# Kernel tuning notes

Measured on AMD Instinct MI355X. Metric: run time of the kernel, lower is better.

The kernel has to match this reference:

```python
import jax, jax.numpy as jnp
import numpy as np

G, NPG = 256, 128          # graphs per batch, nodes per graph
N = G * NPG                # 32768 total nodes
E = 524288                 # total directed edges; first half 'in', second half 'out'
DIN, D = 128, 256          # input feature dim, hidden dim
R = 200                    # num relations
C = 2                      # num classes
EPS = 1e-5                 # batchnorm eps


def setup_inputs() -> dict:
    key = jax.random.key(0)
    ks = jax.random.split(key, 20)

    def w(k, shape):
        fan_in = shape[-2] if len(shape) >= 2 else shape[-1]
        return jax.random.normal(k, shape, jnp.float32) / np.float32(np.sqrt(fan_in))

    return {
        "x": jax.random.normal(ks[0], (N, DIN), jnp.float32),
        "rel_emb": w(ks[1], (R, DIN)),
        # conv1: DIN -> D
        "w_in1": w(ks[2], (DIN, D)), "w_out1": w(ks[3], (DIN, D)),
        "w_loop1": w(ks[4], (DIN, D)), "w_rel1": w(ks[5], (DIN, D)),
        "loop_rel1": w(ks[6], (1, DIN)),
        "bias1": jnp.zeros((D,), jnp.float32),
        "gamma1": jnp.ones((D,), jnp.float32), "beta1": jnp.zeros((D,), jnp.float32),
        # conv2..conv5 stacked: D -> D
        "W_in": w(ks[7], (4, D, D)), "W_out": w(ks[8], (4, D, D)),
        "W_loop": w(ks[9], (4, D, D)), "W_rel": w(ks[10], (4, D, D)),
        "Loop_rel": w(ks[11], (4, 1, D)),
        "Bias": jnp.zeros((4, D), jnp.float32),
        "Gamma": jnp.ones((4, D), jnp.float32), "Beta": jnp.zeros((4, D), jnp.float32),
        # head: concat2 => Linear(4*D, C)
        "lin_w": w(ks[12], (4 * D, C)), "lin_b": jnp.zeros((C,), jnp.float32),
        # graph data (int constants)
        "edge_index": jax.random.randint(ks[13], (2, E), 0, N),
        "edge_type": jax.random.randint(ks[14], (E,), 0, R),
        "batch": jnp.repeat(jnp.arange(G, dtype=jnp.int32), NPG),
        "rel_labels": jax.random.randint(ks[15], (G,), 0, R),
    }


def _compgcn_conv(x, rel, edge_index, edge_type,
                  w_in, w_out, w_loop, w_rel, loop_rel, bias, gamma, beta):
    """One CompGCNConv layer (opn='mult', dropout=identity/eval, BN with batch stats)."""
    n = x.shape[0]
    half = edge_index.shape[1] // 2

    def direction(idx, etype, W):
        src, dst = idx[0], idx[1]
        # symmetric normalization: deg^{-1/2}[src] * deg^{-1/2}[dst]
        deg = jax.ops.segment_sum(jnp.ones_like(src, jnp.float32), src, num_segments=n)
        dinv = jnp.where(deg > 0, deg ** -0.5, 0.0)
        norm = dinv[src] * dinv[dst]                       # [half]
        msg = ((x[src] * rel[etype]) @ W) * norm[:, None]  # [half, D]
        return jax.ops.segment_sum(msg, dst, num_segments=n)

    in_res = direction(edge_index[:, :half], edge_type[:half], w_in)
    out_res = direction(edge_index[:, half:], edge_type[half:], w_out)
    loop_res = (x * loop_rel) @ w_loop                     # self-loop, loop relation, no norm

    out = (in_res + out_res + loop_res) / 3.0 + bias
    mean = out.mean(axis=0)
    var = out.var(axis=0)
    out = (out - mean) / jnp.sqrt(var + EPS) * gamma + beta
    return jax.nn.relu(out), rel @ w_rel


def reference(x, rel_emb, w_in1, w_out1, w_loop1, w_rel1, loop_rel1, bias1, gamma1, beta1,
              W_in, W_out, W_loop, W_rel, Loop_rel, Bias, Gamma, Beta,
              lin_w, lin_b, edge_index, edge_type, batch, rel_labels):
    x, r = _compgcn_conv(x, rel_emb, edge_index, edge_type,
                         w_in1, w_out1, w_loop1, w_rel1, loop_rel1, bias1, gamma1, beta1)
    for l in range(4):  # conv2..conv5 (fixed small layer loop)
        x, r = _compgcn_conv(x, r, edge_index, edge_type,
                             W_in[l], W_out[l], W_loop[l], W_rel[l],
                             Loop_rel[l], Bias[l], Gamma[l], Beta[l])

    # per-graph head/tail nodes (first two nodes of each graph) via segment offsets
    counts = jax.ops.segment_sum(jnp.ones((x.shape[0],), jnp.float32), batch, num_segments=G)
    offsets = (jnp.cumsum(counts) - counts).astype(jnp.int32)
    h_batch = x[offsets]
    t_batch = x[offsets + 1]

    pooled = jax.ops.segment_sum(x, batch, num_segments=G) / counts[:, None]
    rel_embs = r[rel_labels]

    feats = jnp.concatenate([pooled, rel_embs, h_batch, t_batch], axis=1)  # concat2 path
    return feats @ lin_w + lin_b


if __name__ == "__main__":
    out = reference(**setup_inputs())
    print(out.shape, out.dtype)
```

## Files before the change

### kernel.cpp

```cpp
#include <hip/hip_runtime.h>

#define NN 32768
#define GG 256
#define NPGN 128
#define ET 524288
#define EH 262144
#define D1 128
#define D2 256
#define RR 200

typedef unsigned short u16;
typedef __attribute__((ext_vector_type(8))) short bf16x8;
typedef __attribute__((ext_vector_type(4))) float f32x4;
typedef __attribute__((ext_vector_type(8))) unsigned short u16x8;
typedef __attribute__((ext_vector_type(4))) unsigned short u16x4;

__device__ __forceinline__ float bf2f(u16 u) {
    union { unsigned int i; float f; } v; v.i = ((unsigned int)u) << 16; return v.f;
}
__device__ __forceinline__ u16 f2bf(float f) {
    union { unsigned int i; float f; } v; v.f = f;
    unsigned int x = v.i;
    return (u16)((x + 0x7fffu + ((x >> 16) & 1u)) >> 16);
}

__global__ void k_hist(const int* __restrict__ ei, int* __restrict__ hs_in,
                       int* __restrict__ hs_out, int* __restrict__ hd_in,
                       int* __restrict__ hd_out) {
    int e = blockIdx.x * blockDim.x + threadIdx.x;
    if (e >= ET) return;
    int s = ei[e], d = ei[ET + e];
    if (e < EH) { atomicAdd(&hs_in[s], 1);  atomicAdd(&hd_in[d], 1); }
    else        { atomicAdd(&hs_out[s], 1); atomicAdd(&hd_out[d], 1); }
}

__global__ void k_dinv(const int* __restrict__ hs_in, const int* __restrict__ hs_out,
                       float* __restrict__ dinv_in, float* __restrict__ dinv_out) {
    int n = blockIdx.x * blockDim.x + threadIdx.x;
    if (n >= NN) return;
    int a = hs_in[n], b = hs_out[n];
    dinv_in[n]  = a > 0 ? rsqrtf((float)a) : 0.f;
    dinv_out[n] = b > 0 ? rsqrtf((float)b) : 0.f;
}

__global__ __launch_bounds__(1024) void k_scan(const int* __restrict__ hist,
                                               int* __restrict__ off) {
    __shared__ int lds[1024];
    int t = threadIdx.x;
    int base = t * 32;
    int loc[32];
    int s = 0;
#pragma unroll
    for (int i = 0; i < 32; ++i) { loc[i] = s; s += hist[base + i]; }
    lds[t] = s;
    int tot = s;
    __syncthreads();
    for (int st = 1; st < 1024; st <<= 1) {
        int v = (t >= st) ? lds[t - st] : 0;
        __syncthreads();
        lds[t] += v;
        __syncthreads();
    }
    int excl = lds[t] - tot;
#pragma unroll
    for (int i = 0; i < 32; ++i) off[base + i] = excl + loc[i];
    if (t == 1023) off[NN] = lds[1023];
}

__global__ void k_fill(const int* __restrict__ ei, const int* __restrict__ et,
                       const float* __restrict__ dinv, const int* __restrict__ off,
                       int* __restrict__ cur, int* __restrict__ c_src,
                       int* __restrict__ c_et, float* __restrict__ c_norm, int eoff) {
    int e = blockIdx.x * blockDim.x + threadIdx.x;
    if (e >= EH) return;
    int s = ei[eoff + e], d = ei[ET + eoff + e], t = et[eoff + e];
    int slot = off[d] + atomicAdd(&cur[d], 1);
    c_src[slot] = s;
    c_et[slot] = t;
    c_norm[slot] = dinv[s] * dinv[d];
}

__global__ void k_convx(const float* __restrict__ in, u16* __restrict__ out, int n) {
    int i = blockIdx.x * blockDim.x + threadIdx.x;
    if (i < n) out[i] = f2bf(in[i]);
}

__global__ void k_prepw(const float* __restrict__ Wi, const float* __restrict__ Wo,
                        const float* __restrict__ Wl, const float* __restrict__ lr,
                        u16* __restrict__ WiT, u16* __restrict__ WoT,
                        u16* __restrict__ WlT, int K, int L) {
    int idx = blockIdx.x * blockDim.x + threadIdx.x;
    int per = L * K * 256;
    if (idx >= 3 * per) return;
    int fam = idx / per, rem = idx % per;
    int l = rem / (K * 256), rr = rem % (K * 256);
    int k = rr / 256, n = rr % 256;
    const float* src = fam == 0 ? Wi : fam == 1 ? Wo : Wl;
    float v = src[((size_t)l * K + k) * 256 + n];
    if (fam == 2) v *= lr[l * K + k];
    u16* dst = fam == 0 ? WiT : fam == 1 ? WoT : WlT;
    dst[((size_t)l * 256 + n) * K + k] = f2bf(v);
}

template <int K>
__global__ __launch_bounds__(256) void k_gather2(
    const u16* __restrict__ x, const u16* __restrict__ relb,
    const int* __restrict__ csI, const int* __restrict__ cetI,
    const float* __restrict__ cnI, const int* __restrict__ offI,
    const int* __restrict__ csO, const int* __restrict__ cetO,
    const float* __restrict__ cnO, const int* __restrict__ offO,
    u16* __restrict__ aggI, u16* __restrict__ aggO) {
    constexpr int LPN = K / 8;
    constexpr int NPB = 256 / LPN;
    const int dir = blockIdx.y;
    const int* __restrict__ cs  = dir ? csO : csI;
    const int* __restrict__ cet = dir ? cetO : cetI;
    const float* __restrict__ cn = dir ? cnO : cnI;
    const int* __restrict__ off = dir ? offO : offI;
    u16* __restrict__ agg = dir ? aggO : aggI;

    int node = blockIdx.x * NPB + (threadIdx.x / LPN);
    int lane = threadIdx.x % LPN;
    int c = lane * 8;
    int e0 = off[node], e1 = off[node + 1];
    float acc[8] = {};
    int e = e0;
    for (; e + 4 <= e1; e += 4) {
        int s0 = cs[e],     s1 = cs[e + 1], s2 = cs[e + 2], s3 = cs[e + 3];
        int t0 = cet[e],    t1 = cet[e + 1], t2 = cet[e + 2], t3 = cet[e + 3];
        float n0 = cn[e], n1 = cn[e + 1], n2 = cn[e + 2], n3 = cn[e + 3];
        u16x8 xa = *(const u16x8*)(x + (size_t)s0 * K + c);
        u16x8 xb = *(const u16x8*)(x + (size_t)s1 * K + c);
        u16x8 xc = *(const u16x8*)(x + (size_t)s2 * K + c);
        u16x8 xd = *(const u16x8*)(x + (size_t)s3 * K + c);
        u16x8 ra = *(const u16x8*)(relb + (size_t)t0 * K + c);
        u16x8 rb = *(const u16x8*)(relb + (size_t)t1 * K + c);
        u16x8 rc = *(const u16x8*)(relb + (size_t)t2 * K + c);
        u16x8 rd = *(const u16x8*)(relb + (size_t)t3 * K + c);
#pragma unroll
        for (int i = 0; i < 8; ++i)
            acc[i] += n0 * bf2f(xa[i]) * bf2f(ra[i]) + n1 * bf2f(xb[i]) * bf2f(rb[i])
                    + n2 * bf2f(xc[i]) * bf2f(rc[i]) + n3 * bf2f(xd[i]) * bf2f(rd[i]);
    }
    for (; e < e1; ++e) {
        int s0 = cs[e], t0 = cet[e]; float n0 = cn[e];
        u16x8 xa = *(const u16x8*)(x + (size_t)s0 * K + c);
        u16x8 ra = *(const u16x8*)(relb + (size_t)t0 * K + c);
#pragma unroll
        for (int i = 0; i < 8; ++i) acc[i] += n0 * bf2f(xa[i]) * bf2f(ra[i]);
    }
    u16x8 o;
#pragma unroll
    for (int i = 0; i < 8; ++i) o[i] = f2bf(acc[i]);
    *(u16x8*)(agg + (size_t)node * K + c) = o;
}

__device__ __forceinline__ void stage_tile(const u16* __restrict__ src, int baseRow,
                                           int K, int kk, u16* lds, int wave, int lane) {
#pragma unroll
    for (int i = 0; i < 2; ++i) {
        int chunk = wave * 2 + i;
        int row = chunk * 16 + (lane >> 2);
        const u16* g = src + (size_t)(baseRow + row) * K + kk + (lane & 3) * 8;
        u16* l = lds + chunk * 512;
        __builtin_amdgcn_global_load_lds((const __attribute__((address_space(1))) void*)g,
                                         (__attribute__((address_space(3))) void*)l,
                                         16, 0, 0);
    }
}

template <int K>
__global__ __launch_bounds__(256) void k_gemm_mfma(
    const u16* __restrict__ A1, const u16* __restrict__ A2, const u16* __restrict__ A3,
    const u16* __restrict__ W1, const u16* __restrict__ W2, const u16* __restrict__ W3,
    const float* __restrict__ bias, float* __restrict__ C, float* __restrict__ bnsums) {
    __shared__ u16 As_s[2][128 * 32];
    __shared__ u16 Ws_s[2][128 * 32];
    const int tid = threadIdx.x;
    const int wave = tid >> 6, lane = tid & 63;
    const int q = lane >> 4, r = lane & 15;
    const int rowBlk = blockIdx.x * 128;
    const int colBlk = blockIdx.y * 128;
    const int rowBase = rowBlk + (wave & 1) * 64;
    const int colBase = colBlk + (wave >> 1) * 64;

    f32x4 zero = {0.f, 0.f, 0.f, 0.f};
    f32x4 acc[4][4];
#pragma unroll
    for (int i = 0; i < 4; ++i)
#pragma unroll
        for (int j = 0; j < 4; ++j) acc[i][j] = zero;

    const u16* As[3] = {A1, A2, A3};
    const u16* Ws[3] = {W1, W2, W3};
    constexpr int SPS = K / 32;
    constexpr int TOT = 3 * SPS;

    stage_tile(As[0], rowBlk, K, 0, As_s[0], wave, lane);
    stage_tile(Ws[0], colBlk, K, 0, Ws_s[0], wave, lane);

    for (int s = 0; s < TOT; ++s) {
        __syncthreads();
        if (s + 1 < TOT) {
            int seg = (s + 1) / SPS;
            int kk  = ((s + 1) % SPS) * 32;
            stage_tile(As[seg], rowBlk, K, kk, As_s[(s + 1) & 1], wave, lane);
            stage_tile(Ws[seg], colBlk, K, kk, Ws_s[(s + 1) & 1], wave, lane);
        }
        const u16* al = As_s[s & 1] + (wave & 1) * 64 * 32;
        const u16* wl = Ws_s[s & 1] + (wave >> 1) * 64 * 32;
        bf16x8 a[4], b[4];
#pragma unroll
        for (int t = 0; t < 4; ++t) {
            a[t] = *(const bf16x8*)(al + (t * 16 + r) * 32 + q * 8);
            b[t] = *(const bf16x8*)(wl + (t * 16 + r) * 32 + q * 8);
        }
#pragma unroll
        for (int tm = 0; tm < 4; ++tm)
#pragma unroll
            for (int tn = 0; tn < 4; ++tn)
                acc[tm][tn] = __builtin_amdgcn_mfma_f32_16x16x32_bf16(
                    a[tm], b[tn], acc[tm][tn], 0, 0, 0);
    }

#pragma unroll
    for (int tn = 0; tn < 4; ++tn) {
        int col = colBase + tn * 16 + r;
        float bv = bias[col];
        float sv = 0.f, qv = 0.f;
#pragma unroll
        for (int tm = 0; tm < 4; ++tm) {
#pragma unroll
            for (int reg = 0; reg < 4; ++reg) {
                int row = rowBase + tm * 16 + q * 4 + reg;
                float v = acc[tm][tn][reg] / 3.0f + bv;
                C[(size_t)row * 256 + col] = v;
                sv += v; qv += v * v;
            }
        }
        sv += __shfl_xor(sv, 16); sv += __shfl_xor(sv, 32);
        qv += __shfl_xor(qv, 16); qv += __shfl_xor(qv, 32);
        if (q == 0) {
            atomicAdd(&bnsums[col], sv);
            atomicAdd(&bnsums[256 + col], qv);
        }
    }
}

__global__ __launch_bounds__(256) void k_gemm_rel(
    const float* __restrict__ A, const float* __restrict__ W,
    float* __restrict__ C, u16* __restrict__ Cb, int M, int K) {
    __shared__ float As[16][68];
    __shared__ float Wshm[16][68];
    const int tid = threadIdx.x;
    const int tx = tid & 15, ty = tid >> 4;
    const int arow = tid >> 2;
    const int akc  = (tid & 3) << 2;
    const int wk   = tid >> 4;
    const int wn0  = (tid & 15) << 2;
    const int rowBase = blockIdx.x << 6;
    const int colBase = blockIdx.y << 6;
    float acc[4][4] = {};
    for (int k0 = 0; k0 < K; k0 += 16) {
        float4 av = make_float4(0.f, 0.f, 0.f, 0.f);
        int rr = rowBase + arow;
        if (rr < M) av = *(const float4*)(A + (size_t)rr * K + k0 + akc);
        As[akc + 0][arow] = av.x;
        As[akc + 1][arow] = av.y;
        As[akc + 2][arow] = av.z;
        As[akc + 3][arow] = av.w;
        float4 wv = *(const float4*)(W + (size_t)(k0 + wk) * D2 + colBase + wn0);
        Wshm[wk][wn0 + 0] = wv.x;
        Wshm[wk][wn0 + 1] = wv.y;
        Wshm[wk][wn0 + 2] = wv.z;
        Wshm[wk][wn0 + 3] = wv.w;
        __syncthreads();
#pragma unroll
        for (int kk = 0; kk < 16; ++kk) {
            float a0 = As[kk][(ty << 2) + 0], a1 = As[kk][(ty << 2) + 1];
            float a2 = As[kk][(ty << 2) + 2], a3 = As[kk][(ty << 2) + 3];
            float w0 = Wshm[kk][(tx << 2) + 0], w1 = Wshm[kk][(tx << 2) + 1];
            float w2 = Wshm[kk][(tx << 2) + 2], w3 = Wshm[kk][(tx << 2) + 3];
            acc[0][0] += a0 * w0; acc[0][1] += a0 * w1; acc[0][2] += a0 * w2; acc[0][3] += a0 * w3;
            acc[1][0] += a1 * w0; acc[1][1] += a1 * w1; acc[1][2] += a1 * w2; acc[1][3] += a1 * w3;
            acc[2][0] += a2 * w0; acc[2][1] += a2 * w1; acc[2][2] += a2 * w2; acc[2][3] += a2 * w3;
            acc[3][0] += a3 * w0; acc[3][1] += a3 * w1; acc[3][2] += a3 * w2; acc[3][3] += a3 * w3;
        }
        __syncthreads();
    }
#pragma unroll
    for (int i = 0; i < 4; ++i) {
        int rr = rowBase + (ty << 2) + i;
        if (rr >= M) continue;
        float* cp = C + (size_t)rr * D2 + colBase + (tx << 2);
        u16* cb = Cb + (size_t)rr * D2 + colBase + (tx << 2);
        cp[0] = acc[i][0]; cp[1] = acc[i][1]; cp[2] = acc[i][2]; cp[3] = acc[i][3];
        cb[0] = f2bf(acc[i][0]); cb[1] = f2bf(acc[i][1]);
        cb[2] = f2bf(acc[i][2]); cb[3] = f2bf(acc[i][3]);
    }
}

__global__ void k_bnapply(const float4* __restrict__ h4, const float* __restrict__ sums,
                          const float* __restrict__ gamma, const float* __restrict__ beta,
                          u16x4* __restrict__ xb4) {
    int idx = blockIdx.x * blockDim.x + threadIdx.x;
    int f0 = (idx & 63) << 2;
    float4 v = h4[idx];
    u16x4 o;
    float vv[4] = {v.x, v.y, v.z, v.w};
#pragma unroll
    for (int i = 0; i < 4; ++i) {
        int f = f0 + i;
        float mean = sums[f] * (1.0f / NN);
        float var  = sums[256 + f] * (1.0f / NN) - mean * mean;
        float inv  = 1.0f / sqrtf(var + 1e-5f);
        float t = (vv[i] - mean) * inv * gamma[f] + beta[f];
        o[i] = f2bf(t > 0.f ? t : 0.f);
    }
    xb4[idx] = o;
}

__global__ void k_feats(const u16* __restrict__ x, const float* __restrict__ rel,
                        const int* __restrict__ rel_labels, float* __restrict__ feats) {
    int g = blockIdx.x, f = threadIdx.x;
    const u16* xg = x + (size_t)g * NPGN * D2;
    float s = 0.f;
#pragma unroll 8
    for (int n = 0; n < NPGN; ++n) s += bf2f(xg[(size_t)n * D2 + f]);
    float* fg = feats + (size_t)g * 1024;
    fg[f]       = s * (1.0f / NPGN);
    fg[256 + f] = rel[(size_t)rel_labels[g] * D2 + f];
    fg[512 + f] = bf2f(xg[f]);
    fg[768 + f] = bf2f(xg[D2 + f]);
}

__global__ void k_head(const float* __restrict__ feats, const float* __restrict__ lw,
                       const float* __restrict__ lb, float* __restrict__ out) {
    int g = blockIdx.x, t = threadIdx.x;
    __shared__ float s0[256], s1[256];
    float a0 = 0.f, a1 = 0.f;
#pragma unroll
    for (int j = 0; j < 4; ++j) {
        int k = t * 4 + j;
        float fv = feats[(size_t)g * 1024 + k];
        a0 += fv * lw[k * 2 + 0];
        a1 += fv * lw[k * 2 + 1];
    }
    s0[t] = a0; s1[t] = a1;
    __syncthreads();
    for (int s = 128; s > 0; s >>= 1) {
        if (t < s) { s0[t] += s0[t + s]; s1[t] += s1[t + s]; }
        __syncthreads();
    }
    if (t == 0) {
        out[g * 2 + 0] = s0[0] + lb[0];
        out[g * 2 + 1] = s1[0] + lb[1];
    }
}

extern "C" void kernel_launch(void* const* d_in, const int* in_sizes, int n_in,
                              void* d_out, int out_size, void* d_ws, size_t ws_size,
                              hipStream_t stream) {
    const float* x0   = (const float*)d_in[0];
    const float* rel0 = (const float*)d_in[1];
    const int* edge_index = (const int*)d_in[20];
    const int* edge_type  = (const int*)d_in[21];
    const int* rel_labels = (const int*)d_in[23];
    float* out = (float*)d_out;

    float* ws = (float*)d_ws;
    float* h     = ws;
    float* relA  = h + (size_t)NN * 256;
    float* relB  = relA + (size_t)RR * 256;
    float* dinv_in  = relB + (size_t)RR * 256;
    float* dinv_out = dinv_in + NN;
    float* cnorm_in  = dinv_out + NN;
    float* cnorm_out = cnorm_in + EH;
    float* bnsums    = cnorm_out + EH;
    float* feats     = bnsums + 512;
    int* csrc_in  = (int*)(feats + GG * 1024);
    int* cet_in   = csrc_in + EH;
    int* csrc_out = cet_in + EH;
    int* cet_out  = csrc_out + EH;
    int* off_in   = cet_out + EH;
    int* off_out  = off_in + NN + 8;
    int* hs_in    = off_out + NN + 8;
    int* hs_out   = hs_in + NN;
    int* hd_in    = hs_out + NN;
    int* hd_out   = hd_in + NN;
    int* cur_in   = hd_out + NN;
    int* cur_out  = cur_in + NN;
    u16* xbf0 = (u16*)(cur_out + NN);
    u16* xbfA = xbf0 + (size_t)NN * 128;
    u16* aggI = xbfA + (size_t)NN * 256;
    u16* aggO = aggI + (size_t)NN * 256;
    u16* wt0  = aggO + (size_t)NN * 256;
    u16* wtS  = wt0 + 3 * 256 * 128;
    u16* relbf = wtS + 12 * 65536;

    hipMemsetAsync(hs_in, 0, 6 * NN * sizeof(int), stream);
    k_hist<<<ET / 256, 256, 0, stream>>>(edge_index, hs_in, hs_out, hd_in, hd_out);
    k_dinv<<<NN / 256, 256, 0, stream>>>(hs_in, hs_out, dinv_in, dinv_out);
    k_scan<<<1, 1024, 0, stream>>>(hd_in, off_in);
    k_scan<<<1, 1024, 0, stream>>>(hd_out, off_out);
    k_fill<<<EH / 256, 256, 0, stream>>>(edge_index, edge_type, dinv_in, off_in,
                                         cur_in, csrc_in, cet_in, cnorm_in, 0);
    k_fill<<<EH / 256, 256, 0, stream>>>(edge_index, edge_type, dinv_out, off_out,
                                         cur_out, csrc_out, cet_out, cnorm_out, EH);
    k_convx<<<(NN * D1) / 256, 256, 0, stream>>>(x0, xbf0, NN * D1);
    k_convx<<<(RR * D1 + 255) / 256, 256, 0, stream>>>(rel0, relbf, RR * D1);
    k_prepw<<<(3 * D1 * 256) / 256, 256, 0, stream>>>(
        (const float*)d_in[2], (const float*)d_in[3], (const float*)d_in[4],
        (const float*)d_in[6], wt0, wt0 + 256 * D1, wt0 + 2 * 256 * D1, D1, 1);
    k_prepw<<<(3 * 4 * D2 * 256) / 256, 256, 0, stream>>>(
        (const float*)d_in[10], (const float*)d_in[11], (const float*)d_in[12],
        (const float*)d_in[14], wtS, wtS + 4 * 65536, wtS + 8 * 65536, D2, 4);

    const float* rc = rel0; float* rn = relA;

    for (int l = 0; l < 5; ++l) {
        const int K = (l == 0) ? D1 : D2;
        const u16* xb = (l == 0) ? xbf0 : xbfA;
        const u16 *WiT, *WoT, *WlT;
        const float *Wr, *bias, *gamma, *beta;
        if (l == 0) {
            WiT = wt0; WoT = wt0 + 256 * D1; WlT = wt0 + 2 * 256 * D1;
            Wr = (const float*)d_in[5];
            bias  = (const float*)d_in[7];
            gamma = (const float*)d_in[8];
            beta  = (const float*)d_in[9];
        } else {
            int m = l - 1;
            WiT = wtS + (size_t)m * 65536;
            WoT = wtS + (size_t)(4 + m) * 65536;
            WlT = wtS + (size_t)(8 + m) * 65536;
            Wr = (const float*)d_in[13] + (size_t)m * D2 * D2;
            bias  = (const float*)d_in[15] + (size_t)m * D2;
            gamma = (const float*)d_in[16] + (size_t)m * D2;
            beta  = (const float*)d_in[17] + (size_t)m * D2;
        }

        if (K == D1) {
            dim3 ggr(NN / 16, 2);
            k_gather2<D1><<<ggr, 256, 0, stream>>>(xb, relbf, csrc_in, cet_in,
                cnorm_in, off_in, csrc_out, cet_out, cnorm_out, off_out, aggI, aggO);
        } else {
            dim3 ggr(NN / 8, 2);
            k_gather2<D2><<<ggr, 256, 0, stream>>>(xb, relbf, csrc_in, cet_in,
                cnorm_in, off_in, csrc_out, cet_out, cnorm_out, off_out, aggI, aggO);
        }
        hipMemsetAsync(bnsums, 0, 512 * sizeof(float), stream);
        dim3 ggrid(NN / 128, 2);
        if (K == D1) k_gemm_mfma<D1><<<ggrid, 256, 0, stream>>>(aggI, aggO, xb, WiT, WoT, WlT, bias, h, bnsums);
        else         k_gemm_mfma<D2><<<ggrid, 256, 0, stream>>>(aggI, aggO, xb, WiT, WoT, WlT, bias, h, bnsums);
        k_bnapply<<<(NN * 256 / 4) / 256, 256, 0, stream>>>((const float4*)h, bnsums,
                                                            gamma, beta, (u16x4*)xbfA);
        k_gemm_rel<<<dim3(4, 4), 256, 0, stream>>>(rc, Wr, rn, relbf, RR, K);
        const float* nr = rn;
        rn = (l == 0) ? relB : (float*)rc;
        rc = nr;
    }

    k_feats<<<GG, 256, 0, stream>>>(xbfA, rc, rel_labels, feats);
    k_head<<<GG, 256, 0, stream>>>(feats, (const float*)d_in[18],
                                   (const float*)d_in[19], out);
}
```

Before: 829.5 us.

## Degree-sort CSR nodes, split gather over columns, shrink GEMM tile, store bf16 pre-BN

```diff
diff --git a/kernel.cpp b/kernel.cpp
--- a/kernel.cpp
+++ b/kernel.cpp
@@ -13,7 +13,6 @@
 typedef __attribute__((ext_vector_type(8))) short bf16x8;
 typedef __attribute__((ext_vector_type(4))) float f32x4;
 typedef __attribute__((ext_vector_type(8))) unsigned short u16x8;
-typedef __attribute__((ext_vector_type(4))) unsigned short u16x4;
 
 __device__ __forceinline__ float bf2f(u16 u) {
     union { unsigned int i; float f; } v; v.i = ((unsigned int)u) << 16; return v.f;
@@ -41,6 +40,44 @@
     int a = hs_in[n], b = hs_out[n];
     dinv_in[n]  = a > 0 ? rsqrtf((float)a) : 0.f;
     dinv_out[n] = b > 0 ? rsqrtf((float)b) : 0.f;
+}
+
+__global__ void k_deghist(const int* __restrict__ hdI, const int* __restrict__ hdO,
+                          int* __restrict__ dh) {
+    int n = blockIdx.x * blockDim.x + threadIdx.x;
+    if (n >= NN) return;
+    atomicAdd(&dh[min(hdI[n], 63)], 1);
+    atomicAdd(&dh[64 + min(hdO[n], 63)], 1);
+}
+
+__global__ void k_scan64(const int* __restrict__ dh, int* __restrict__ dstart) {
+    int dir = threadIdx.x;
+    if (dir >= 2) return;
+    int s = 0;
+    for (int i = 0; i < 64; ++i) { dstart[dir * 64 + i] = s; s += dh[dir * 64 + i]; }
+}
+
+__global__ void k_place(const int* __restrict__ hdI, const int* __restrict__ hdO,
+                        const int* __restrict__ dstart, int* __restrict__ dcur,
+                        int* __restrict__ permI, int* __restrict__ permO,
+                        int* __restrict__ rankI, int* __restrict__ rankO) {
+    int n = blockIdx.x * blockDim.x + threadIdx.x;
+    if (n >= NN) return;
+    int dI = min(hdI[n], 63);
+    int rI = dstart[dI] + atomicAdd(&dcur[dI], 1);
+    permI[rI] = n; rankI[n] = rI;
+    int dO = min(hdO[n], 63);
+    int rO = dstart[64 + dO] + atomicAdd(&dcur[64 + dO], 1);
+    permO[rO] = n; rankO[n] = rO;
+}
+
+__global__ void k_degsorted(const int* __restrict__ permI, const int* __restrict__ permO,
+                            const int* __restrict__ hdI, const int* __restrict__ hdO,
+                            int* __restrict__ degSI, int* __restrict__ degSO) {
+    int i = blockIdx.x * blockDim.x + threadIdx.x;
+    if (i >= NN) return;
+    degSI[i] = hdI[permI[i]];
+    degSO[i] = hdO[permO[i]];
 }
 
 __global__ __launch_bounds__(1024) void k_scan(const int* __restrict__ hist,
@@ -68,13 +105,14 @@
 }
 
 __global__ void k_fill(const int* __restrict__ ei, const int* __restrict__ et,
-                       const float* __restrict__ dinv, const int* __restrict__ off,
-                       int* __restrict__ cur, int* __restrict__ c_src,
-                       int* __restrict__ c_et, float* __restrict__ c_norm, int eoff) {
+                       const float* __restrict__ dinv, const int* __restrict__ offS,
+                       const int* __restrict__ rank, int* __restrict__ cur,
+                       int* __restrict__ c_src, int* __restrict__ c_et,
+                       float* __restrict__ c_norm, int eoff) {
     int e = blockIdx.x * blockDim.x + threadIdx.x;
     if (e >= EH) return;
     int s = ei[eoff + e], d = ei[ET + eoff + e], t = et[eoff + e];
-    int slot = off[d] + atomicAdd(&cur[d], 1);
+    int slot = offS[rank[d]] + atomicAdd(&cur[d], 1);
     c_src[slot] = s;
     c_et[slot] = t;
     c_norm[slot] = dinv[s] * dinv[d];
@@ -103,31 +141,33 @@
 }
 
 template <int K>
-__global__ __launch_bounds__(256) void k_gather2(
+__global__ __launch_bounds__(256) void k_gather4(
     const u16* __restrict__ x, const u16* __restrict__ relb,
     const int* __restrict__ csI, const int* __restrict__ cetI,
     const float* __restrict__ cnI, const int* __restrict__ offI,
     const int* __restrict__ csO, const int* __restrict__ cetO,
     const float* __restrict__ cnO, const int* __restrict__ offO,
-    u16* __restrict__ aggI, u16* __restrict__ aggO) {
-    constexpr int LPN = K / 8;
-    constexpr int NPB = 256 / LPN;
+    const int* __restrict__ permI, const int* __restrict__ permO,
+    u16* __restrict__ aggI, u16* __restrict__ aggO, float* __restrict__ bnsums) {
+    if (blockIdx.x == 0 && blockIdx.y == 0 && blockIdx.z == 0 && threadIdx.x < 128)
+        ((float4*)bnsums)[threadIdx.x] = make_float4(0.f, 0.f, 0.f, 0.f);
     const int dir = blockIdx.y;
-    const int* __restrict__ cs  = dir ? csO : csI;
-    const int* __restrict__ cet = dir ? cetO : cetI;
+    const int* __restrict__ cs   = dir ? csO : csI;
+    const int* __restrict__ cet  = dir ? cetO : cetI;
     const float* __restrict__ cn = dir ? cnO : cnI;
-    const int* __restrict__ off = dir ? offO : offI;
+    const int* __restrict__ off  = dir ? offO : offI;
+    const int* __restrict__ perm = dir ? permO : permI;
     u16* __restrict__ agg = dir ? aggO : aggI;
 
-    int node = blockIdx.x * NPB + (threadIdx.x / LPN);
-    int lane = threadIdx.x % LPN;
-    int c = lane * 8;
-    int e0 = off[node], e1 = off[node + 1];
+    int idx = blockIdx.x * 32 + (threadIdx.x >> 3);
+    int node = perm[idx];
+    int c = blockIdx.z * 64 + (threadIdx.x & 7) * 8;
+    int e0 = off[idx], e1 = off[idx + 1];
     float acc[8] = {};
     int e = e0;
     for (; e + 4 <= e1; e += 4) {
-        int s0 = cs[e],     s1 = cs[e + 1], s2 = cs[e + 2], s3 = cs[e + 3];
-        int t0 = cet[e],    t1 = cet[e + 1], t2 = cet[e + 2], t3 = cet[e + 3];
+        int s0 = cs[e],  s1 = cs[e + 1],  s2 = cs[e + 2],  s3 = cs[e + 3];
+        int t0 = cet[e], t1 = cet[e + 1], t2 = cet[e + 2], t3 = cet[e + 3];
         float n0 = cn[e], n1 = cn[e + 1], n2 = cn[e + 2], n3 = cn[e + 3];
         u16x8 xa = *(const u16x8*)(x + (size_t)s0 * K + c);
         u16x8 xb = *(const u16x8*)(x + (size_t)s1 * K + c);
@@ -155,39 +195,35 @@
     *(u16x8*)(agg + (size_t)node * K + c) = o;
 }
 
-__device__ __forceinline__ void stage_tile(const u16* __restrict__ src, int baseRow,
-                                           int K, int kk, u16* lds, int wave, int lane) {
-#pragma unroll
-    for (int i = 0; i < 2; ++i) {
-        int chunk = wave * 2 + i;
-        int row = chunk * 16 + (lane >> 2);
-        const u16* g = src + (size_t)(baseRow + row) * K + kk + (lane & 3) * 8;
-        u16* l = lds + chunk * 512;
-        __builtin_amdgcn_global_load_lds((const __attribute__((address_space(1))) void*)g,
-                                         (__attribute__((address_space(3))) void*)l,
-                                         16, 0, 0);
-    }
+__device__ __forceinline__ void stage16(const u16* __restrict__ src, int baseRow,
+                                        int K, int kk, u16* lds, int chunk, int lane) {
+    int row = chunk * 16 + (lane >> 2);
+    int ks  = (lane & 3) ^ ((lane >> 2) & 3);
+    const u16* g = src + (size_t)(baseRow + row) * K + kk + ks * 8;
+    __builtin_amdgcn_global_load_lds((const __attribute__((address_space(1))) void*)g,
+                                     (__attribute__((address_space(3))) void*)(lds + chunk * 512),
+                                     16, 0, 0);
 }
 
 template <int K>
-__global__ __launch_bounds__(256) void k_gemm_mfma(
+__global__ __launch_bounds__(256, 4) void k_gemm_mfma(
     const u16* __restrict__ A1, const u16* __restrict__ A2, const u16* __restrict__ A3,
     const u16* __restrict__ W1, const u16* __restrict__ W2, const u16* __restrict__ W3,
-    const float* __restrict__ bias, float* __restrict__ C, float* __restrict__ bnsums) {
-    __shared__ u16 As_s[2][128 * 32];
+    const float* __restrict__ bias, u16* __restrict__ hb, float* __restrict__ bnsums) {
+    __shared__ u16 As_s[2][64 * 32];
     __shared__ u16 Ws_s[2][128 * 32];
     const int tid = threadIdx.x;
     const int wave = tid >> 6, lane = tid & 63;
     const int q = lane >> 4, r = lane & 15;
-    const int rowBlk = blockIdx.x * 128;
+    const int rowBlk = blockIdx.x * 64;
     const int colBlk = blockIdx.y * 128;
-    const int rowBase = rowBlk + (wave & 1) * 64;
+    const int rowBase = rowBlk + (wave & 1) * 32;
     const int colBase = colBlk + (wave >> 1) * 64;
 
     f32x4 zero = {0.f, 0.f, 0.f, 0.f};
-    f32x4 acc[4][4];
-#pragma unroll
-    for (int i = 0; i < 4; ++i)
+    f32x4 acc[2][4];
+#pragma unroll
+    for (int i = 0; i < 2; ++i)
 #pragma unroll
         for (int j = 0; j < 4; ++j) acc[i][j] = zero;
 
@@ -196,27 +232,29 @@
     constexpr int SPS = K / 32;
     constexpr int TOT = 3 * SPS;
 
-    stage_tile(As[0], rowBlk, K, 0, As_s[0], wave, lane);
-    stage_tile(Ws[0], colBlk, K, 0, Ws_s[0], wave, lane);
-
+    stage16(As[0], rowBlk, K, 0, As_s[0], wave, lane);
+    stage16(Ws[0], colBlk, K, 0, Ws_s[0], 2 * wave, lane);
+    stage16(Ws[0], colBlk, K, 0, Ws_s[0], 2 * wave + 1, lane);
+
+    const int sw = (q ^ (r & 3)) * 8;
     for (int s = 0; s < TOT; ++s) {
         __syncthreads();
         if (s + 1 < TOT) {
             int seg = (s + 1) / SPS;
             int kk  = ((s + 1) % SPS) * 32;
-            stage_tile(As[seg], rowBlk, K, kk, As_s[(s + 1) & 1], wave, lane);
-            stage_tile(Ws[seg], colBlk, K, kk, Ws_s[(s + 1) & 1], wave, lane);
+            stage16(As[seg], rowBlk, K, kk, As_s[(s + 1) & 1], wave, lane);
+            stage16(Ws[seg], colBlk, K, kk, Ws_s[(s + 1) & 1], 2 * wave, lane);
+            stage16(Ws[seg], colBlk, K, kk, Ws_s[(s + 1) & 1], 2 * wave + 1, lane);
         }
-        const u16* al = As_s[s & 1] + (wave & 1) * 64 * 32;
+        const u16* al = As_s[s & 1] + (wave & 1) * 32 * 32;
         const u16* wl = Ws_s[s & 1] + (wave >> 1) * 64 * 32;
-        bf16x8 a[4], b[4];
-#pragma unroll
-        for (int t = 0; t < 4; ++t) {
-            a[t] = *(const bf16x8*)(al + (t * 16 + r) * 32 + q * 8);
-            b[t] = *(const bf16x8*)(wl + (t * 16 + r) * 32 + q * 8);
-        }
-#pragma unroll
-        for (int tm = 0; tm < 4; ++tm)
+        bf16x8 a[2], b[4];
+#pragma unroll
+        for (int t = 0; t < 2; ++t) a[t] = *(const bf16x8*)(al + (t * 16 + r) * 32 + sw);
+#pragma unroll
+        for (int t = 0; t < 4; ++t) b[t] = *(const bf16x8*)(wl + (t * 16 + r) * 32 + sw);
+#pragma unroll
+        for (int tm = 0; tm < 2; ++tm)
 #pragma unroll
             for (int tn = 0; tn < 4; ++tn)
                 acc[tm][tn] = __builtin_amdgcn_mfma_f32_16x16x32_bf16(
@@ -229,12 +267,12 @@
         float bv = bias[col];
         float sv = 0.f, qv = 0.f;
 #pragma unroll
-        for (int tm = 0; tm < 4; ++tm) {
+        for (int tm = 0; tm < 2; ++tm) {
 #pragma unroll
             for (int reg = 0; reg < 4; ++reg) {
                 int row = rowBase + tm * 16 + q * 4 + reg;
-                float v = acc[tm][tn][reg] / 3.0f + bv;
-                C[(size_t)row * 256 + col] = v;
+                float v = acc[tm][tn][reg] * (1.0f / 3.0f) + bv;
+                hb[(size_t)row * 256 + col] = f2bf(v);
                 sv += v; qv += v * v;
             }
         }
@@ -300,24 +338,23 @@
     }
 }
 
-__global__ void k_bnapply(const float4* __restrict__ h4, const float* __restrict__ sums,
+__global__ void k_bnapply(const u16x8* __restrict__ hb8, const float* __restrict__ sums,
                           const float* __restrict__ gamma, const float* __restrict__ beta,
-                          u16x4* __restrict__ xb4) {
+                          u16x8* __restrict__ xb8) {
     int idx = blockIdx.x * blockDim.x + threadIdx.x;
-    int f0 = (idx & 63) << 2;
-    float4 v = h4[idx];
-    u16x4 o;
-    float vv[4] = {v.x, v.y, v.z, v.w};
-#pragma unroll
-    for (int i = 0; i < 4; ++i) {
+    int f0 = (idx & 31) << 3;
+    u16x8 v = hb8[idx];
+    u16x8 o;
+#pragma unroll
+    for (int i = 0; i < 8; ++i) {
         int f = f0 + i;
         float mean = sums[f] * (1.0f / NN);
         float var  = sums[256 + f] * (1.0f / NN) - mean * mean;
         float inv  = 1.0f / sqrtf(var + 1e-5f);
-        float t = (vv[i] - mean) * inv * gamma[f] + beta[f];
+        float t = (bf2f(v[i]) - mean) * inv * gamma[f] + beta[f];
         o[i] = f2bf(t > 0.f ? t : 0.f);
     }
-    xb4[idx] = o;
+    xb8[idx] = o;
 }
 
 __global__ void k_feats(const u16* __restrict__ x, const float* __restrict__ rel,
@@ -369,8 +406,7 @@
     float* out = (float*)d_out;
 
     float* ws = (float*)d_ws;
-    float* h     = ws;
-    float* relA  = h + (size_t)NN * 256;
+    float* relA  = ws;
     float* relB  = relA + (size_t)RR * 256;
     float* dinv_in  = relB + (size_t)RR * 256;
     float* dinv_out = dinv_in + NN;
@@ -382,31 +418,46 @@
     int* cet_in   = csrc_in + EH;
     int* csrc_out = cet_in + EH;
     int* cet_out  = csrc_out + EH;
-    int* off_in   = cet_out + EH;
-    int* off_out  = off_in + NN + 8;
-    int* hs_in    = off_out + NN + 8;
+    int* offS_in  = cet_out + EH;
+    int* offS_out = offS_in + NN + 8;
+    int* permI    = offS_out + NN + 8;
+    int* permO    = permI + NN;
+    int* rankI    = permO + NN;
+    int* rankO    = rankI + NN;
+    int* degSI    = rankO + NN;
+    int* degSO    = degSI + NN;
+    int* dstart   = degSO + NN;
+    int* hs_in    = dstart + 128;
     int* hs_out   = hs_in + NN;
     int* hd_in    = hs_out + NN;
     int* hd_out   = hd_in + NN;
     int* cur_in   = hd_out + NN;
     int* cur_out  = cur_in + NN;
-    u16* xbf0 = (u16*)(cur_out + NN);
+    int* dh       = cur_out + NN;
+    int* dcur     = dh + 128;
+    u16* xbf0 = (u16*)(dcur + 128);
     u16* xbfA = xbf0 + (size_t)NN * 128;
     u16* aggI = xbfA + (size_t)NN * 256;
     u16* aggO = aggI + (size_t)NN * 256;
-    u16* wt0  = aggO + (size_t)NN * 256;
+    u16* hb   = aggO + (size_t)NN * 256;
+    u16* wt0  = hb + (size_t)NN * 256;
     u16* wtS  = wt0 + 3 * 256 * 128;
     u16* relbf = wtS + 12 * 65536;
 
-    hipMemsetAsync(hs_in, 0, 6 * NN * sizeof(int), stream);
+    hipMemsetAsync(hs_in, 0, (6 * NN + 256) * sizeof(int), stream);
     k_hist<<<ET / 256, 256, 0, stream>>>(edge_index, hs_in, hs_out, hd_in, hd_out);
     k_dinv<<<NN / 256, 256, 0, stream>>>(hs_in, hs_out, dinv_in, dinv_out);
-    k_scan<<<1, 1024, 0, stream>>>(hd_in, off_in);
-    k_scan<<<1, 1024, 0, stream>>>(hd_out, off_out);
-    k_fill<<<EH / 256, 256, 0, stream>>>(edge_index, edge_type, dinv_in, off_in,
-                                         cur_in, csrc_in, cet_in, cnorm_in, 0);
-    k_fill<<<EH / 256, 256, 0, stream>>>(edge_index, edge_type, dinv_out, off_out,
-                                         cur_out, csrc_out, cet_out, cnorm_out, EH);
+    k_deghist<<<NN / 256, 256, 0, stream>>>(hd_in, hd_out, dh);
+    k_scan64<<<1, 64, 0, stream>>>(dh, dstart);
+    k_place<<<NN / 256, 256, 0, stream>>>(hd_in, hd_out, dstart, dcur,
+                                          permI, permO, rankI, rankO);
+    k_degsorted<<<NN / 256, 256, 0, stream>>>(permI, permO, hd_in, hd_out, degSI, degSO);
+    k_scan<<<1, 1024, 0, stream>>>(degSI, offS_in);
+    k_scan<<<1, 1024, 0, stream>>>(degSO, offS_out);
+    k_fill<<<EH / 256, 256, 0, stream>>>(edge_index, edge_type, dinv_in, offS_in,
+                                         rankI, cur_in, csrc_in, cet_in, cnorm_in, 0);
+    k_fill<<<EH / 256, 256, 0, stream>>>(edge_index, edge_type, dinv_out, offS_out,
+                                         rankO, cur_out, csrc_out, cet_out, cnorm_out, EH);
     k_convx<<<(NN * D1) / 256, 256, 0, stream>>>(x0, xbf0, NN * D1);
     k_convx<<<(RR * D1 + 255) / 256, 256, 0, stream>>>(rel0, relbf, RR * D1);
     k_prepw<<<(3 * D1 * 256) / 256, 256, 0, stream>>>(
@@ -440,21 +491,18 @@
             beta  = (const float*)d_in[17] + (size_t)m * D2;
         }
 
-        if (K == D1) {
-            dim3 ggr(NN / 16, 2);
-            k_gather2<D1><<<ggr, 256, 0, stream>>>(xb, relbf, csrc_in, cet_in,
-                cnorm_in, off_in, csrc_out, cet_out, cnorm_out, off_out, aggI, aggO);
-        } else {
-            dim3 ggr(NN / 8, 2);
-            k_gather2<D2><<<ggr, 256, 0, stream>>>(xb, relbf, csrc_in, cet_in,
-                cnorm_in, off_in, csrc_out, cet_out, cnorm_out, off_out, aggI, aggO);
-        }
-        hipMemsetAsync(bnsums, 0, 512 * sizeof(float), stream);
-        dim3 ggrid(NN / 128, 2);
-        if (K == D1) k_gemm_mfma<D1><<<ggrid, 256, 0, stream>>>(aggI, aggO, xb, WiT, WoT, WlT, bias, h, bnsums);
-        else         k_gemm_mfma<D2><<<ggrid, 256, 0, stream>>>(aggI, aggO, xb, WiT, WoT, WlT, bias, h, bnsums);
-        k_bnapply<<<(NN * 256 / 4) / 256, 256, 0, stream>>>((const float4*)h, bnsums,
-                                                            gamma, beta, (u16x4*)xbfA);
+        dim3 ggr(NN / 32, 2, K / 64);
+        if (K == D1) k_gather4<D1><<<ggr, 256, 0, stream>>>(xb, relbf,
+            csrc_in, cet_in, cnorm_in, offS_in, csrc_out, cet_out, cnorm_out, offS_out,
+            permI, permO, aggI, aggO, bnsums);
+        else         k_gather4<D2><<<ggr, 256, 0, stream>>>(xb, relbf,
+            csrc_in, cet_in, cnorm_in, offS_in, csrc_out, cet_out, cnorm_out, offS_out,
+            permI, permO, aggI, aggO, bnsums);
+        dim3 ggrid(NN / 64, 2);
+        if (K == D1) k_gemm_mfma<D1><<<ggrid, 256, 0, stream>>>(aggI, aggO, xb, WiT, WoT, WlT, bias, hb, bnsums);
+        else         k_gemm_mfma<D2><<<ggrid, 256, 0, stream>>>(aggI, aggO, xb, WiT, WoT, WlT, bias, hb, bnsums);
+        k_bnapply<<<(NN * 256 / 8) / 256, 256, 0, stream>>>((const u16x8*)hb, bnsums,
+                                                            gamma, beta, (u16x8*)xbfA);
         k_gemm_rel<<<dim3(4, 4), 256, 0, stream>>>(rc, Wr, rn, relbf, RR, K);
         const float* nr = rn;
         rn = (l == 0) ? relB : (float*)rc;
```

Measured after the change: 1.314 ms. +58.4%, slower.

## Store GEMM output as bf16, swizzle LDS tiles, fold bnsums zeroing into gather

Applied to the files above, without the earlier changes.

```diff
diff --git a/kernel.cpp b/kernel.cpp
--- a/kernel.cpp
+++ b/kernel.cpp
@@ -13,7 +13,6 @@
 typedef __attribute__((ext_vector_type(8))) short bf16x8;
 typedef __attribute__((ext_vector_type(4))) float f32x4;
 typedef __attribute__((ext_vector_type(8))) unsigned short u16x8;
-typedef __attribute__((ext_vector_type(4))) unsigned short u16x4;
 
 __device__ __forceinline__ float bf2f(u16 u) {
     union { unsigned int i; float f; } v; v.i = ((unsigned int)u) << 16; return v.f;
@@ -109,7 +108,9 @@
     const float* __restrict__ cnI, const int* __restrict__ offI,
     const int* __restrict__ csO, const int* __restrict__ cetO,
     const float* __restrict__ cnO, const int* __restrict__ offO,
-    u16* __restrict__ aggI, u16* __restrict__ aggO) {
+    u16* __restrict__ aggI, u16* __restrict__ aggO, float* __restrict__ bnsums) {
+    if (blockIdx.x == 0 && blockIdx.y == 0 && threadIdx.x < 128)
+        ((float4*)bnsums)[threadIdx.x] = make_float4(0.f, 0.f, 0.f, 0.f);
     constexpr int LPN = K / 8;
     constexpr int NPB = 256 / LPN;
     const int dir = blockIdx.y;
@@ -126,8 +127,8 @@
     float acc[8] = {};
     int e = e0;
     for (; e + 4 <= e1; e += 4) {
-        int s0 = cs[e],     s1 = cs[e + 1], s2 = cs[e + 2], s3 = cs[e + 3];
-        int t0 = cet[e],    t1 = cet[e + 1], t2 = cet[e + 2], t3 = cet[e + 3];
+        int s0 = cs[e],  s1 = cs[e + 1],  s2 = cs[e + 2],  s3 = cs[e + 3];
+        int t0 = cet[e], t1 = cet[e + 1], t2 = cet[e + 2], t3 = cet[e + 3];
         float n0 = cn[e], n1 = cn[e + 1], n2 = cn[e + 2], n3 = cn[e + 3];
         u16x8 xa = *(const u16x8*)(x + (size_t)s0 * K + c);
         u16x8 xb = *(const u16x8*)(x + (size_t)s1 * K + c);
@@ -155,25 +156,21 @@
     *(u16x8*)(agg + (size_t)node * K + c) = o;
 }
 
-__device__ __forceinline__ void stage_tile(const u16* __restrict__ src, int baseRow,
-                                           int K, int kk, u16* lds, int wave, int lane) {
-#pragma unroll
-    for (int i = 0; i < 2; ++i) {
-        int chunk = wave * 2 + i;
-        int row = chunk * 16 + (lane >> 2);
-        const u16* g = src + (size_t)(baseRow + row) * K + kk + (lane & 3) * 8;
-        u16* l = lds + chunk * 512;
-        __builtin_amdgcn_global_load_lds((const __attribute__((address_space(1))) void*)g,
-                                         (__attribute__((address_space(3))) void*)l,
-                                         16, 0, 0);
-    }
+__device__ __forceinline__ void stage16(const u16* __restrict__ src, int baseRow,
+                                        int K, int kk, u16* lds, int chunk, int lane) {
+    int row = chunk * 16 + (lane >> 2);
+    int ks  = (lane & 3) ^ ((lane >> 2) & 3);
+    const u16* g = src + (size_t)(baseRow + row) * K + kk + ks * 8;
+    __builtin_amdgcn_global_load_lds((const __attribute__((address_space(1))) void*)g,
+                                     (__attribute__((address_space(3))) void*)(lds + chunk * 512),
+                                     16, 0, 0);
 }
 
 template <int K>
 __global__ __launch_bounds__(256) void k_gemm_mfma(
     const u16* __restrict__ A1, const u16* __restrict__ A2, const u16* __restrict__ A3,
     const u16* __restrict__ W1, const u16* __restrict__ W2, const u16* __restrict__ W3,
-    const float* __restrict__ bias, float* __restrict__ C, float* __restrict__ bnsums) {
+    const float* __restrict__ bias, u16* __restrict__ hb, float* __restrict__ bnsums) {
     __shared__ u16 As_s[2][128 * 32];
     __shared__ u16 Ws_s[2][128 * 32];
     const int tid = threadIdx.x;
@@ -196,24 +193,29 @@
     constexpr int SPS = K / 32;
     constexpr int TOT = 3 * SPS;
 
-    stage_tile(As[0], rowBlk, K, 0, As_s[0], wave, lane);
-    stage_tile(Ws[0], colBlk, K, 0, Ws_s[0], wave, lane);
-
+    stage16(As[0], rowBlk, K, 0, As_s[0], 2 * wave, lane);
+    stage16(As[0], rowBlk, K, 0, As_s[0], 2 * wave + 1, lane);
+    stage16(Ws[0], colBlk, K, 0, Ws_s[0], 2 * wave, lane);
+    stage16(Ws[0], colBlk, K, 0, Ws_s[0], 2 * wave + 1, lane);
+
+    const int sw = (q ^ (r & 3)) * 8;
     for (int s = 0; s < TOT; ++s) {
         __syncthreads();
         if (s + 1 < TOT) {
             int seg = (s + 1) / SPS;
             int kk  = ((s + 1) % SPS) * 32;
-            stage_tile(As[seg], rowBlk, K, kk, As_s[(s + 1) & 1], wave, lane);
-            stage_tile(Ws[seg], colBlk, K, kk, Ws_s[(s + 1) & 1], wave, lane);
+            stage16(As[seg], rowBlk, K, kk, As_s[(s + 1) & 1], 2 * wave, lane);
+            stage16(As[seg], rowBlk, K, kk, As_s[(s + 1) & 1], 2 * wave + 1, lane);
+            stage16(Ws[seg], colBlk, K, kk, Ws_s[(s + 1) & 1], 2 * wave, lane);
+            stage16(Ws[seg], colBlk, K, kk, Ws_s[(s + 1) & 1], 2 * wave + 1, lane);
         }
         const u16* al = As_s[s & 1] + (wave & 1) * 64 * 32;
         const u16* wl = Ws_s[s & 1] + (wave >> 1) * 64 * 32;
         bf16x8 a[4], b[4];
 #pragma unroll
         for (int t = 0; t < 4; ++t) {
-            a[t] = *(const bf16x8*)(al + (t * 16 + r) * 32 + q * 8);
-            b[t] = *(const bf16x8*)(wl + (t * 16 + r) * 32 + q * 8);
+            a[t] = *(const bf16x8*)(al + (t * 16 + r) * 32 + sw);
+            b[t] = *(const bf16x8*)(wl + (t * 16 + r) * 32 + sw);
         }
 #pragma unroll
         for (int tm = 0; tm < 4; ++tm)
@@ -233,8 +235,8 @@
 #pragma unroll
             for (int reg = 0; reg < 4; ++reg) {
                 int row = rowBase + tm * 16 + q * 4 + reg;
-                float v = acc[tm][tn][reg] / 3.0f + bv;
-                C[(size_t)row * 256 + col] = v;
+                float v = acc[tm][tn][reg] * (1.0f / 3.0f) + bv;
+                hb[(size_t)row * 256 + col] = f2bf(v);
                 sv += v; qv += v * v;
             }
         }
@@ -300,24 +302,23 @@
     }
 }
 
-__global__ void k_bnapply(const float4* __restrict__ h4, const float* __restrict__ sums,
+__global__ void k_bnapply(const u16x8* __restrict__ hb8, const float* __restrict__ sums,
                           const float* __restrict__ gamma, const float* __restrict__ beta,
-                          u16x4* __restrict__ xb4) {
+                          u16x8* __restrict__ xb8) {
     int idx = blockIdx.x * blockDim.x + threadIdx.x;
-    int f0 = (idx & 63) << 2;
-    float4 v = h4[idx];
-    u16x4 o;
-    float vv[4] = {v.x, v.y, v.z, v.w};
-#pragma unroll
-    for (int i = 0; i < 4; ++i) {
+    int f0 = (idx & 31) << 3;
+    u16x8 v = hb8[idx];
+    u16x8 o;
+#pragma unroll
+    for (int i = 0; i < 8; ++i) {
         int f = f0 + i;
         float mean = sums[f] * (1.0f / NN);
         float var  = sums[256 + f] * (1.0f / NN) - mean * mean;
         float inv  = 1.0f / sqrtf(var + 1e-5f);
-        float t = (vv[i] - mean) * inv * gamma[f] + beta[f];
+        float t = (bf2f(v[i]) - mean) * inv * gamma[f] + beta[f];
         o[i] = f2bf(t > 0.f ? t : 0.f);
     }
-    xb4[idx] = o;
+    xb8[idx] = o;
 }
 
 __global__ void k_feats(const u16* __restrict__ x, const float* __restrict__ rel,
@@ -369,8 +370,7 @@
     float* out = (float*)d_out;
 
     float* ws = (float*)d_ws;
-    float* h     = ws;
-    float* relA  = h + (size_t)NN * 256;
+    float* relA  = ws;
     float* relB  = relA + (size_t)RR * 256;
     float* dinv_in  = relB + (size_t)RR * 256;
     float* dinv_out = dinv_in + NN;
@@ -394,7 +394,8 @@
     u16* xbfA = xbf0 + (size_t)NN * 128;
     u16* aggI = xbfA + (size_t)NN * 256;
     u16* aggO = aggI + (size_t)NN * 256;
-    u16* wt0  = aggO + (size_t)NN * 256;
+    u16* hb   = aggO + (size_t)NN * 256;
+    u16* wt0  = hb + (size_t)NN * 256;
     u16* wtS  = wt0 + 3 * 256 * 128;
     u16* relbf = wtS + 12 * 65536;
 
@@ -443,18 +444,17 @@
         if (K == D1) {
             dim3 ggr(NN / 16, 2);
             k_gather2<D1><<<ggr, 256, 0, stream>>>(xb, relbf, csrc_in, cet_in,
-                cnorm_in, off_in, csrc_out, cet_out, cnorm_out, off_out, aggI, aggO);
+                cnorm_in, off_in, csrc_out, cet_out, cnorm_out, off_out, aggI, aggO, bnsums);
         } else {
             dim3 ggr(NN / 8, 2);
             k_gather2<D2><<<ggr, 256, 0, stream>>>(xb, relbf, csrc_in, cet_in,
-                cnorm_in, off_in, csrc_out, cet_out, cnorm_out, off_out, aggI, aggO);
-        }
-        hipMemsetAsync(bnsums, 0, 512 * sizeof(float), stream);
+                cnorm_in, off_in, csrc_out, cet_out, cnorm_out, off_out, aggI, aggO, bnsums);
+        }
         dim3 ggrid(NN / 128, 2);
-        if (K == D1) k_gemm_mfma<D1><<<ggrid, 256, 0, stream>>>(aggI, aggO, xb, WiT, WoT, WlT, bias, h, bnsums);
-        else         k_gemm_mfma<D2><<<ggrid, 256, 0, stream>>>(aggI, aggO, xb, WiT, WoT, WlT, bias, h, bnsums);
-        k_bnapply<<<(NN * 256 / 4) / 256, 256, 0, stream>>>((const float4*)h, bnsums,
-                                                            gamma, beta, (u16x4*)xbfA);
+        if (K == D1) k_gemm_mfma<D1><<<ggrid, 256, 0, stream>>>(aggI, aggO, xb, WiT, WoT, WlT, bias, hb, bnsums);
+        else         k_gemm_mfma<D2><<<ggrid, 256, 0, stream>>>(aggI, aggO, xb, WiT, WoT, WlT, bias, hb, bnsums);
+        k_bnapply<<<(NN * 256 / 8) / 256, 256, 0, stream>>>((const u16x8*)hb, bnsums,
+                                                            gamma, beta, (u16x8*)xbfA);
         k_gemm_rel<<<dim3(4, 4), 256, 0, stream>>>(rc, Wr, rn, relbf, RR, K);
         const float* nr = rn;
         rn = (l == 0) ? relB : (float*)rc;
```

After: 812.2 us. 2.1% less time.
